# Performance work log

Measured on AMD Instinct MI355X. Metric: run time of the kernel, lower is better.

The kernel has to match this reference:

```python
import jax, jax.numpy as jnp
import numpy as np

N = 1024
BATCH = 256


def setup_inputs() -> dict:
    key = jax.random.key(0)
    k1, k2 = jax.random.split(key)
    log_alpha = jax.random.normal(k1, (BATCH, N), dtype=jnp.float32)
    W = jax.random.normal(k2, (N, N), dtype=jnp.float32)  # unnormalized transition matrix
    return {"log_alpha": log_alpha, "W": W}


def reference(log_alpha, W):
    # log_softmax over dim=0 (columns are distributions over next state)
    log_T = jax.nn.log_softmax(W, axis=0)  # [N, N]
    # log_domain_matmul: out[i, m] = logsumexp_j( log_T[i, j] + log_alpha[m, j] )
    # then transpose back -> out[m, i]
    # broadcast-add cube [BATCH, N, N] then logsumexp over j (tropical-semiring matmul)
    out = jax.scipy.special.logsumexp(
        log_T[None, :, :] + log_alpha[:, None, :], axis=2
    )  # [BATCH, N]
    return out
```

## Files before the change

kernel.cpp:

```cpp
#include <hip/hip_runtime.h>
#include <hip/hip_bf16.h>

#define N 1024
#define BATCH 256

typedef __attribute__((ext_vector_type(4))) short short4v;
typedef __attribute__((ext_vector_type(8))) short short8;
typedef __attribute__((ext_vector_type(4))) float f32x4;

static __device__ __forceinline__ ushort bfbits(float f) {
    union { __hip_bfloat16 h; ushort u; } cv; cv.h = __float2bfloat16(f); return cv.u;
}
static __device__ __forceinline__ float bf2f(ushort u) {
    union { ushort u; __hip_bfloat16 h; } cv; cv.u = u; return __bfloat162float(cv.h);
}

__global__ __launch_bounds__(256) void k1_psplit(const float* __restrict__ W,
                                                 float* __restrict__ psum,
                                                 ushort* __restrict__ Ph,
                                                 ushort* __restrict__ Pl) {
    const int t = threadIdx.x, lane = t & 63, w = t >> 6;
    const int cg = blockIdx.x & 3, slab = blockIdx.x >> 2;
    const int c = cg * 256 + lane * 4;
    __shared__ f32x4 sm[4][64];
    f32x4 acc = {0.f, 0.f, 0.f, 0.f};
#pragma unroll
    for (int it = 0; it < 4; ++it) {
        const int row = slab * 16 + w * 4 + it;
        const f32x4 v = *(const f32x4*)(W + row * N + c);
        short4v ph, pl;
        f32x4 e;
#pragma unroll
        for (int x = 0; x < 4; ++x) {
            e[x] = __expf(v[x]);
            const ushort h = bfbits(e[x]);
            ph[x] = (short)h;
            pl[x] = (short)bfbits(e[x] - bf2f(h));
        }
        *(short4v*)(Ph + row * N + c) = ph;
        *(short4v*)(Pl + row * N + c) = pl;
        acc += e;
    }
    sm[w][lane] = acc;
    __syncthreads();
    if (t < 64)
        *(f32x4*)(psum + slab * N + c) =
            sm[0][lane] + sm[1][lane] + sm[2][lane] + sm[3][lane];
}

__global__ __launch_bounds__(256) void k2_qsplit(const float* __restrict__ la,
                                                 const float* __restrict__ psum,
                                                 ushort* __restrict__ Qh,
                                                 ushort* __restrict__ Ql) {
    const int t = threadIdx.x;
    const int cg = blockIdx.x & 15, mg = blockIdx.x >> 4;
    const int c0 = cg * 64;
    __shared__ float smred[4][64];
    __shared__ float lcs[64];

    {
        const int col = t & 63, sg = t >> 6;
        float a = 0.f;
#pragma unroll
        for (int i = 0; i < 16; ++i)
            a += psum[(sg * 16 + i) * N + c0 + col];
        smred[sg][col] = a;
    }
    __syncthreads();
    if (t < 64)
        lcs[t] = __logf(smred[0][t] + smred[1][t] + smred[2][t] + smred[3][t]);
    __syncthreads();

    const int row = mg * 16 + (t >> 4);
    const int cc  = (t & 15) * 4;
    const f32x4 v = *(const f32x4*)(la + row * N + c0 + cc);
    short4v qh, ql;
#pragma unroll
    for (int x = 0; x < 4; ++x) {
        const float qv = __expf(v[x] - lcs[cc + x]);
        const ushort h = bfbits(qv);
        qh[x] = (short)h;
        ql[x] = (short)bfbits(qv - bf2f(h));
    }
    *(short4v*)(Qh + row * N + c0 + cc) = qh;
    *(short4v*)(Ql + row * N + c0 + cc) = ql;
}

__global__ __launch_bounds__(512) void k3_mm(const ushort* __restrict__ Qh,
                                             const ushort* __restrict__ Ql,
                                             const ushort* __restrict__ Ph,
                                             const ushort* __restrict__ Pl,
                                             float* __restrict__ out) {
    __shared__ f32x4 red[512];

    const int t    = threadIdx.x;
    const int lane = t & 63;
    const int wid  = t >> 6;
    const int wm   = (wid >> 1) & 1;
    const int wn   = wid & 1;
    const int g    = wid >> 2;
    const int m0   = (blockIdx.x >> 5) * 32;
    const int i0   = (blockIdx.x & 31) * 32;

    const int kb = g * 512 + (lane >> 4) * 8;
    const ushort* pAh = Qh + (m0 + wm * 16 + (lane & 15)) * N + kb;
    const ushort* pAl = Ql + (m0 + wm * 16 + (lane & 15)) * N + kb;
    const ushort* pBh = Ph + (i0 + wn * 16 + (lane & 15)) * N + kb;
    const ushort* pBl = Pl + (i0 + wn * 16 + (lane & 15)) * N + kb;

    short8 rAh[8], rAl[8], rBh[8], rBl[8];
#pragma unroll
    for (int c = 0; c < 8; ++c) {
        rAh[c] = *(const short8*)(pAh + c * 32);
        rAl[c] = *(const short8*)(pAl + c * 32);
        rBh[c] = *(const short8*)(pBh + c * 32);
        rBl[c] = *(const short8*)(pBl + c * 32);
    }

    f32x4 acc0 = {0.f, 0.f, 0.f, 0.f};
    f32x4 acc1 = {0.f, 0.f, 0.f, 0.f};

#pragma unroll
    for (int ks = 0; ks < 16; ++ks) {
        const int c = ks & 7;
        const short8 ah = rAh[c], al = rAl[c], bh = rBh[c], bl = rBl[c];
        if (ks < 8) {
            rAh[c] = *(const short8*)(pAh + (ks + 8) * 32);
            rAl[c] = *(const short8*)(pAl + (ks + 8) * 32);
            rBh[c] = *(const short8*)(pBh + (ks + 8) * 32);
            rBl[c] = *(const short8*)(pBl + (ks + 8) * 32);
        }
        if (ks & 1) {
            acc1 = __builtin_amdgcn_mfma_f32_16x16x32_bf16(ah, bh, acc1, 0, 0, 0);
            acc1 = __builtin_amdgcn_mfma_f32_16x16x32_bf16(ah, bl, acc1, 0, 0, 0);
            acc1 = __builtin_amdgcn_mfma_f32_16x16x32_bf16(al, bh, acc1, 0, 0, 0);
        } else {
            acc0 = __builtin_amdgcn_mfma_f32_16x16x32_bf16(ah, bh, acc0, 0, 0, 0);
            acc0 = __builtin_amdgcn_mfma_f32_16x16x32_bf16(ah, bl, acc0, 0, 0, 0);
            acc0 = __builtin_amdgcn_mfma_f32_16x16x32_bf16(al, bh, acc0, 0, 0, 0);
        }
    }

    red[wid * 64 + lane] = acc0 + acc1;
    __syncthreads();
    if (wid < 4) {
        const f32x4 s = red[wid * 64 + lane] + red[(wid + 4) * 64 + lane];
        const int om = m0 + wm * 16 + (lane >> 4) * 4;
        const int oi = i0 + wn * 16 + (lane & 15);
#pragma unroll
        for (int r = 0; r < 4; ++r)
            out[(om + r) * N + oi] = __logf(s[r]);
    }
}

extern "C" void kernel_launch(void* const* d_in, const int* in_sizes, int n_in,
                              void* d_out, int out_size, void* d_ws, size_t ws_size,
                              hipStream_t stream) {
    const float* la = (const float*)d_in[0];
    const float* W  = (const float*)d_in[1];
    float* out = (float*)d_out;

    char* ws = (char*)d_ws;
    float*  psum = (float*)ws;
    ushort* Ph   = (ushort*)(ws + (256 << 10));
    ushort* Pl   = Ph + (size_t)N * N;
    ushort* Qh   = Pl + (size_t)N * N;
    ushort* Ql   = Qh + (size_t)BATCH * N;

    k1_psplit<<<256, 256, 0, stream>>>(W, psum, Ph, Pl);
    k2_qsplit<<<256, 256, 0, stream>>>(la, psum, Qh, Ql);
    k3_mm<<<256, 512, 0, stream>>>(Qh, Ql, Ph, Pl, out);
}
```

Measured before the change: 78.50 us.

## Fuse three kernels into one persistent kernel with grid-wide atomic barriers

Merges the P-split, column-normalizer and MFMA matmul kernels into a single 256-block launch that synchronizes through two spin-wait atomic barriers in workspace, reset by a memset. The Q operand is no longer written to global memory: each block recomputes exp(log_alpha - lcs) and the bf16 hi/lo split inline before the MFMAs. The matmul tiling also changes to 8 waves each covering a 128-wide K chunk with a 2x2 block of 16x16 tiles, reduced through shared memory. This targets launch gaps and Q round-trip traffic, at the cost of redundant exp work across blocks and a grid barrier that depends on all 256 blocks being co-resident.

```diff
diff --git a/kernel.cpp b/kernel.cpp
--- a/kernel.cpp
+++ b/kernel.cpp
@@ -2,11 +2,12 @@
 #include <hip/hip_bf16.h>
 
 #define N 1024
-#define BATCH 256
+#define NBLK 256
 
 typedef __attribute__((ext_vector_type(4))) short short4v;
 typedef __attribute__((ext_vector_type(8))) short short8;
 typedef __attribute__((ext_vector_type(4))) float f32x4;
+typedef __attribute__((ext_vector_type(8))) float f32x8;
 
 static __device__ __forceinline__ ushort bfbits(float f) {
     union { __hip_bfloat16 h; ushort u; } cv; cv.h = __float2bfloat16(f); return cv.u;
@@ -15,138 +16,133 @@
     union { ushort u; __hip_bfloat16 h; } cv; cv.u = u; return __bfloat162float(cv.h);
 }
 
-__global__ __launch_bounds__(256) void k1_psplit(const float* __restrict__ W,
-                                                 float* __restrict__ psum,
-                                                 ushort* __restrict__ Ph,
-                                                 ushort* __restrict__ Pl) {
-    const int t = threadIdx.x, lane = t & 63, w = t >> 6;
-    const int cg = blockIdx.x & 3, slab = blockIdx.x >> 2;
-    const int c = cg * 256 + lane * 4;
-    __shared__ f32x4 sm[4][64];
-    f32x4 acc = {0.f, 0.f, 0.f, 0.f};
-#pragma unroll
-    for (int it = 0; it < 4; ++it) {
-        const int row = slab * 16 + w * 4 + it;
-        const f32x4 v = *(const f32x4*)(W + row * N + c);
-        short4v ph, pl;
-        f32x4 e;
-#pragma unroll
-        for (int x = 0; x < 4; ++x) {
-            e[x] = __expf(v[x]);
-            const ushort h = bfbits(e[x]);
-            ph[x] = (short)h;
-            pl[x] = (short)bfbits(e[x] - bf2f(h));
-        }
-        *(short4v*)(Ph + row * N + c) = ph;
-        *(short4v*)(Pl + row * N + c) = pl;
-        acc += e;
-    }
-    sm[w][lane] = acc;
-    __syncthreads();
-    if (t < 64)
-        *(f32x4*)(psum + slab * N + c) =
-            sm[0][lane] + sm[1][lane] + sm[2][lane] + sm[3][lane];
-}
+#define MFMA16(a, b, c) __builtin_amdgcn_mfma_f32_16x16x32_bf16(a, b, c, 0, 0, 0)
 
-__global__ __launch_bounds__(256) void k2_qsplit(const float* __restrict__ la,
-                                                 const float* __restrict__ psum,
-                                                 ushort* __restrict__ Qh,
-                                                 ushort* __restrict__ Ql) {
+__global__ __launch_bounds__(512, 2) void fused(const float* __restrict__ la,
+                                                const float* __restrict__ W,
+                                                float* __restrict__ out,
+                                                unsigned* __restrict__ bar,
+                                                float* __restrict__ lcs_g,
+                                                float* __restrict__ psum,
+                                                ushort* __restrict__ Ph,
+                                                ushort* __restrict__ Pl) {
+    __shared__ __align__(16) char smem_raw[8 * 64 * 4 * 16];
     const int t = threadIdx.x;
-    const int cg = blockIdx.x & 15, mg = blockIdx.x >> 4;
-    const int c0 = cg * 64;
-    __shared__ float smred[4][64];
-    __shared__ float lcs[64];
+    const int b = blockIdx.x;
 
     {
-        const int col = t & 63, sg = t >> 6;
-        float a = 0.f;
+        const int cg = b & 15, slab = b >> 4;
+        const int c4 = cg * 64 + (t & 15) * 4;
+        f32x4* smA = (f32x4*)smem_raw;
+        f32x4 part = {0.f, 0.f, 0.f, 0.f};
 #pragma unroll
-        for (int i = 0; i < 16; ++i)
-            a += psum[(sg * 16 + i) * N + c0 + col];
-        smred[sg][col] = a;
-    }
-    __syncthreads();
-    if (t < 64)
-        lcs[t] = __logf(smred[0][t] + smred[1][t] + smred[2][t] + smred[3][t]);
-    __syncthreads();
-
-    const int row = mg * 16 + (t >> 4);
-    const int cc  = (t & 15) * 4;
-    const f32x4 v = *(const f32x4*)(la + row * N + c0 + cc);
-    short4v qh, ql;
+        for (int rr = 0; rr < 2; ++rr) {
+            const int row = slab * 64 + rr * 32 + (t >> 4);
+            const f32x4 v = *(const f32x4*)(W + row * N + c4);
+            short4v ph, pl;
 #pragma unroll
-    for (int x = 0; x < 4; ++x) {
-        const float qv = __expf(v[x] - lcs[cc + x]);
-        const ushort h = bfbits(qv);
-        qh[x] = (short)h;
-        ql[x] = (short)bfbits(qv - bf2f(h));
-    }
-    *(short4v*)(Qh + row * N + c0 + cc) = qh;
-    *(short4v*)(Ql + row * N + c0 + cc) = ql;
-}
-
-__global__ __launch_bounds__(512) void k3_mm(const ushort* __restrict__ Qh,
-                                             const ushort* __restrict__ Ql,
-                                             const ushort* __restrict__ Ph,
-                                             const ushort* __restrict__ Pl,
-                                             float* __restrict__ out) {
-    __shared__ f32x4 red[512];
-
-    const int t    = threadIdx.x;
-    const int lane = t & 63;
-    const int wid  = t >> 6;
-    const int wm   = (wid >> 1) & 1;
-    const int wn   = wid & 1;
-    const int g    = wid >> 2;
-    const int m0   = (blockIdx.x >> 5) * 32;
-    const int i0   = (blockIdx.x & 31) * 32;
-
-    const int kb = g * 512 + (lane >> 4) * 8;
-    const ushort* pAh = Qh + (m0 + wm * 16 + (lane & 15)) * N + kb;
-    const ushort* pAl = Ql + (m0 + wm * 16 + (lane & 15)) * N + kb;
-    const ushort* pBh = Ph + (i0 + wn * 16 + (lane & 15)) * N + kb;
-    const ushort* pBl = Pl + (i0 + wn * 16 + (lane & 15)) * N + kb;
-
-    short8 rAh[8], rAl[8], rBh[8], rBl[8];
+            for (int x = 0; x < 4; ++x) {
+                const float e = __expf(v[x]);
+                const ushort h = bfbits(e);
+                ph[x] = (short)h;
+                pl[x] = (short)bfbits(e - bf2f(h));
+                part[x] += e;
+            }
+            *(short4v*)(Ph + row * N + c4) = ph;
+            *(short4v*)(Pl + row * N + c4) = pl;
+        }
+        smA[(t >> 4) * 16 + (t & 15)] = part;
+        __syncthreads();
+        if (t < 16) {
+            f32x4 s = smA[t];
 #pragma unroll
-    for (int c = 0; c < 8; ++c) {
-        rAh[c] = *(const short8*)(pAh + c * 32);
-        rAl[c] = *(const short8*)(pAl + c * 32);
-        rBh[c] = *(const short8*)(pBh + c * 32);
-        rBl[c] = *(const short8*)(pBl + c * 32);
-    }
-
-    f32x4 acc0 = {0.f, 0.f, 0.f, 0.f};
-    f32x4 acc1 = {0.f, 0.f, 0.f, 0.f};
-
-#pragma unroll
-    for (int ks = 0; ks < 16; ++ks) {
-        const int c = ks & 7;
-        const short8 ah = rAh[c], al = rAl[c], bh = rBh[c], bl = rBl[c];
-        if (ks < 8) {
-            rAh[c] = *(const short8*)(pAh + (ks + 8) * 32);
-            rAl[c] = *(const short8*)(pAl + (ks + 8) * 32);
-            rBh[c] = *(const short8*)(pBh + (ks + 8) * 32);
-            rBl[c] = *(const short8*)(pBl + (ks + 8) * 32);
-        }
-        if (ks & 1) {
-            acc1 = __builtin_amdgcn_mfma_f32_16x16x32_bf16(ah, bh, acc1, 0, 0, 0);
-            acc1 = __builtin_amdgcn_mfma_f32_16x16x32_bf16(ah, bl, acc1, 0, 0, 0);
-            acc1 = __builtin_amdgcn_mfma_f32_16x16x32_bf16(al, bh, acc1, 0, 0, 0);
-        } else {
-            acc0 = __builtin_amdgcn_mfma_f32_16x16x32_bf16(ah, bh, acc0, 0, 0, 0);
-            acc0 = __builtin_amdgcn_mfma_f32_16x16x32_bf16(ah, bl, acc0, 0, 0, 0);
-            acc0 = __builtin_amdgcn_mfma_f32_16x16x32_bf16(al, bh, acc0, 0, 0, 0);
+            for (int g = 1; g < 32; ++g) s += smA[g * 16 + t];
+            *(f32x4*)(psum + slab * N + cg * 64 + t * 4) = s;
         }
     }
 
-    red[wid * 64 + lane] = acc0 + acc1;
+    __syncthreads();
+    if (t == 0) {
+        __threadfence();
+        atomicAdd(&bar[0], 1u);
+        while (atomicAdd(&bar[0], 0u) < NBLK) __builtin_amdgcn_s_sleep(8);
+        __threadfence();
+    }
+    __syncthreads();
+
+    if (b < 16 && t < 64) {
+        const int c = b * 64 + t;
+        float s = 0.f;
+#pragma unroll
+        for (int sl = 0; sl < 16; ++sl) s += psum[sl * N + c];
+        lcs_g[c] = __logf(s);
+    }
+
+    __syncthreads();
+    if (t == 0) {
+        __threadfence();
+        atomicAdd(&bar[1], 1u);
+        while (atomicAdd(&bar[1], 0u) < NBLK) __builtin_amdgcn_s_sleep(8);
+        __threadfence();
+    }
+    __syncthreads();
+
+    const int lane = t & 63, wid = t >> 6;
+    const int fr = lane & 15, q = lane >> 4;
+    const int m0 = (b >> 5) * 32, i0 = (b & 31) * 32;
+    const int kc = wid * 128;
+
+    const float*  plA0 = la + (m0 + fr) * N;
+    const float*  plA1 = la + (m0 + 16 + fr) * N;
+    const ushort* pB0h = Ph + (i0 + fr) * N;
+    const ushort* pB1h = Ph + (i0 + 16 + fr) * N;
+    const ushort* pB0l = Pl + (i0 + fr) * N;
+    const ushort* pB1l = Pl + (i0 + 16 + fr) * N;
+
+    f32x4 a00 = {0.f,0.f,0.f,0.f}, a01 = {0.f,0.f,0.f,0.f};
+    f32x4 a10 = {0.f,0.f,0.f,0.f}, a11 = {0.f,0.f,0.f,0.f};
+
+#pragma unroll
+    for (int s = 0; s < 4; ++s) {
+        const int kk = kc + s * 32 + q * 8;
+        const f32x8 v0   = *(const f32x8*)(plA0 + kk);
+        const f32x8 v1   = *(const f32x8*)(plA1 + kk);
+        const f32x8 vlc  = *(const f32x8*)(lcs_g + kk);
+        const short8 b0h = *(const short8*)(pB0h + kk);
+        const short8 b1h = *(const short8*)(pB1h + kk);
+        const short8 b0l = *(const short8*)(pB0l + kk);
+        const short8 b1l = *(const short8*)(pB1l + kk);
+        short8 a0h, a0l, a1h, a1l;
+#pragma unroll
+        for (int x = 0; x < 8; ++x) {
+            const float q0 = __expf(v0[x] - vlc[x]);
+            const ushort h0 = bfbits(q0);
+            a0h[x] = (short)h0;
+            a0l[x] = (short)bfbits(q0 - bf2f(h0));
+            const float q1 = __expf(v1[x] - vlc[x]);
+            const ushort h1 = bfbits(q1);
+            a1h[x] = (short)h1;
+            a1l[x] = (short)bfbits(q1 - bf2f(h1));
+        }
+        a00 = MFMA16(a0h, b0h, a00); a00 = MFMA16(a0h, b0l, a00); a00 = MFMA16(a0l, b0h, a00);
+        a01 = MFMA16(a0h, b1h, a01); a01 = MFMA16(a0h, b1l, a01); a01 = MFMA16(a0l, b1h, a01);
+        a10 = MFMA16(a1h, b0h, a10); a10 = MFMA16(a1h, b0l, a10); a10 = MFMA16(a1l, b0h, a10);
+        a11 = MFMA16(a1h, b1h, a11); a11 = MFMA16(a1h, b1l, a11); a11 = MFMA16(a1l, b1h, a11);
+    }
+
+    __syncthreads();
+    f32x4* red = (f32x4*)smem_raw;
+    red[(wid * 64 + lane) * 4 + 0] = a00;
+    red[(wid * 64 + lane) * 4 + 1] = a01;
+    red[(wid * 64 + lane) * 4 + 2] = a10;
+    red[(wid * 64 + lane) * 4 + 3] = a11;
     __syncthreads();
     if (wid < 4) {
-        const f32x4 s = red[wid * 64 + lane] + red[(wid + 4) * 64 + lane];
-        const int om = m0 + wm * 16 + (lane >> 4) * 4;
-        const int oi = i0 + wn * 16 + (lane & 15);
+        f32x4 s = red[lane * 4 + wid];
+#pragma unroll
+        for (int w2 = 1; w2 < 8; ++w2) s += red[(w2 * 64 + lane) * 4 + wid];
+        const int om = m0 + (wid >> 1) * 16 + q * 4;
+        const int oi = i0 + (wid & 1) * 16 + fr;
 #pragma unroll
         for (int r = 0; r < 4; ++r)
             out[(om + r) * N + oi] = __logf(s[r]);
@@ -161,13 +157,12 @@
     float* out = (float*)d_out;
 
     char* ws = (char*)d_ws;
-    float*  psum = (float*)ws;
-    ushort* Ph   = (ushort*)(ws + (256 << 10));
-    ushort* Pl   = Ph + (size_t)N * N;
-    ushort* Qh   = Pl + (size_t)N * N;
-    ushort* Ql   = Qh + (size_t)BATCH * N;
+    unsigned* bar = (unsigned*)ws;
+    float* lcs_g  = (float*)(ws + 4096);
+    float* psum   = (float*)(ws + 8192);
+    ushort* Ph    = (ushort*)(ws + (128 << 10));
+    ushort* Pl    = Ph + (size_t)N * N;
 
-    k1_psplit<<<256, 256, 0, stream>>>(W, psum, Ph, Pl);
-    k2_qsplit<<<256, 256, 0, stream>>>(la, psum, Qh, Ql);
-    k3_mm<<<256, 512, 0, stream>>>(Qh, Ql, Ph, Pl, out);
+    hipMemsetAsync(bar, 0, 256, stream);
+    fused<<<NBLK, 512, 0, stream>>>(la, W, out, bar, lcs_g, psum, Ph, Pl);
 }
```

New measurement: 98.07 us. +24.9%, slower.

## Stage matmul operand tiles in LDS and share A/B fragments across waves

Applied to the files above, without the earlier changes.

The k3 matmul now copies 32x256 chunks of Qh/Ql/Ph/Pl into padded shared-memory tiles with register prefetch of the next chunk, instead of each wave loading its own fragments straight from global memory. Waves are reorganized so each covers both 16-row M halves for one N half over a 64-wide K slice, with a 4-way K-split reduction at the end. The aim is to cut redundant global/L2 traffic and raise MFMA work per loaded operand. In exchange it adds LDS traffic, two barriers per K chunk, and a larger final reduction.

```diff
diff --git a/kernel.cpp b/kernel.cpp
--- a/kernel.cpp
+++ b/kernel.cpp
@@ -3,6 +3,7 @@
 
 #define N 1024
 #define BATCH 256
+#define LP 264
 
 typedef __attribute__((ext_vector_type(4))) short short4v;
 typedef __attribute__((ext_vector_type(8))) short short8;
@@ -14,6 +15,8 @@
 static __device__ __forceinline__ float bf2f(ushort u) {
     union { ushort u; __hip_bfloat16 h; } cv; cv.u = u; return __bfloat162float(cv.h);
 }
+
+#define MFMA16(a, b, c) __builtin_amdgcn_mfma_f32_16x16x32_bf16(a, b, c, 0, 0, 0)
 
 __global__ __launch_bounds__(256) void k1_psplit(const float* __restrict__ W,
                                                  float* __restrict__ psum,
@@ -91,62 +94,84 @@
                                              const ushort* __restrict__ Ph,
                                              const ushort* __restrict__ Pl,
                                              float* __restrict__ out) {
-    __shared__ f32x4 red[512];
+    __shared__ ushort sQh[32 * LP], sQl[32 * LP];
+    __shared__ ushort sPh[32 * LP], sPl[32 * LP];
 
     const int t    = threadIdx.x;
     const int lane = t & 63;
     const int wid  = t >> 6;
-    const int wm   = (wid >> 1) & 1;
     const int wn   = wid & 1;
-    const int g    = wid >> 2;
+    const int g    = wid >> 1;
     const int m0   = (blockIdx.x >> 5) * 32;
     const int i0   = (blockIdx.x & 31) * 32;
 
-    const int kb = g * 512 + (lane >> 4) * 8;
-    const ushort* pAh = Qh + (m0 + wm * 16 + (lane & 15)) * N + kb;
-    const ushort* pAl = Ql + (m0 + wm * 16 + (lane & 15)) * N + kb;
-    const ushort* pBh = Ph + (i0 + wn * 16 + (lane & 15)) * N + kb;
-    const ushort* pBl = Pl + (i0 + wn * 16 + (lane & 15)) * N + kb;
+    const int srow = t >> 4;
+    const int skc  = (t & 15) * 8;
+    const ushort* gQh = Qh + (m0 + srow) * N + skc;
+    const ushort* gQl = Ql + (m0 + srow) * N + skc;
+    const ushort* gPh = Ph + (i0 + srow) * N + skc;
+    const ushort* gPl = Pl + (i0 + srow) * N + skc;
+    const int sd0 = srow * LP + skc;
+    const int sd1 = sd0 + 128;
 
-    short8 rAh[8], rAl[8], rBh[8], rBl[8];
-#pragma unroll
-    for (int c = 0; c < 8; ++c) {
-        rAh[c] = *(const short8*)(pAh + c * 32);
-        rAl[c] = *(const short8*)(pAl + c * 32);
-        rBh[c] = *(const short8*)(pBh + c * 32);
-        rBl[c] = *(const short8*)(pBl + c * 32);
-    }
+    const int fr  = lane & 15;
+    const int fkb = g * 64 + (lane >> 4) * 8;
+    const int a0off = (fr) * LP + fkb;
+    const int a1off = (16 + fr) * LP + fkb;
+    const int boff  = (wn * 16 + fr) * LP + fkb;
 
     f32x4 acc0 = {0.f, 0.f, 0.f, 0.f};
     f32x4 acc1 = {0.f, 0.f, 0.f, 0.f};
 
+    short8 vqh0 = *(const short8*)(gQh),       vqh1 = *(const short8*)(gQh + 128);
+    short8 vql0 = *(const short8*)(gQl),       vql1 = *(const short8*)(gQl + 128);
+    short8 vph0 = *(const short8*)(gPh),       vph1 = *(const short8*)(gPh + 128);
+    short8 vpl0 = *(const short8*)(gPl),       vpl1 = *(const short8*)(gPl + 128);
+
+    for (int k0 = 0; k0 < N; k0 += 256) {
+        __syncthreads();
+        *(short8*)&sQh[sd0] = vqh0;  *(short8*)&sQh[sd1] = vqh1;
+        *(short8*)&sQl[sd0] = vql0;  *(short8*)&sQl[sd1] = vql1;
+        *(short8*)&sPh[sd0] = vph0;  *(short8*)&sPh[sd1] = vph1;
+        *(short8*)&sPl[sd0] = vpl0;  *(short8*)&sPl[sd1] = vpl1;
+        if (k0 + 256 < N) {
+            vqh0 = *(const short8*)(gQh + k0 + 256);  vqh1 = *(const short8*)(gQh + k0 + 384);
+            vql0 = *(const short8*)(gQl + k0 + 256);  vql1 = *(const short8*)(gQl + k0 + 384);
+            vph0 = *(const short8*)(gPh + k0 + 256);  vph1 = *(const short8*)(gPh + k0 + 384);
+            vpl0 = *(const short8*)(gPl + k0 + 256);  vpl1 = *(const short8*)(gPl + k0 + 384);
+        }
+        __syncthreads();
 #pragma unroll
-    for (int ks = 0; ks < 16; ++ks) {
-        const int c = ks & 7;
-        const short8 ah = rAh[c], al = rAl[c], bh = rBh[c], bl = rBl[c];
-        if (ks < 8) {
-            rAh[c] = *(const short8*)(pAh + (ks + 8) * 32);
-            rAl[c] = *(const short8*)(pAl + (ks + 8) * 32);
-            rBh[c] = *(const short8*)(pBh + (ks + 8) * 32);
-            rBl[c] = *(const short8*)(pBl + (ks + 8) * 32);
-        }
-        if (ks & 1) {
-            acc1 = __builtin_amdgcn_mfma_f32_16x16x32_bf16(ah, bh, acc1, 0, 0, 0);
-            acc1 = __builtin_amdgcn_mfma_f32_16x16x32_bf16(ah, bl, acc1, 0, 0, 0);
-            acc1 = __builtin_amdgcn_mfma_f32_16x16x32_bf16(al, bh, acc1, 0, 0, 0);
-        } else {
-            acc0 = __builtin_amdgcn_mfma_f32_16x16x32_bf16(ah, bh, acc0, 0, 0, 0);
-            acc0 = __builtin_amdgcn_mfma_f32_16x16x32_bf16(ah, bl, acc0, 0, 0, 0);
-            acc0 = __builtin_amdgcn_mfma_f32_16x16x32_bf16(al, bh, acc0, 0, 0, 0);
+        for (int ks = 0; ks < 2; ++ks) {
+            const int so = ks * 32;
+            const short8 bh  = *(const short8*)&sPh[boff + so];
+            const short8 bl  = *(const short8*)&sPl[boff + so];
+            const short8 ah0 = *(const short8*)&sQh[a0off + so];
+            const short8 al0 = *(const short8*)&sQl[a0off + so];
+            const short8 ah1 = *(const short8*)&sQh[a1off + so];
+            const short8 al1 = *(const short8*)&sQl[a1off + so];
+            acc0 = MFMA16(ah0, bh, acc0);
+            acc0 = MFMA16(ah0, bl, acc0);
+            acc0 = MFMA16(al0, bh, acc0);
+            acc1 = MFMA16(ah1, bh, acc1);
+            acc1 = MFMA16(ah1, bl, acc1);
+            acc1 = MFMA16(al1, bh, acc1);
         }
     }
 
-    red[wid * 64 + lane] = acc0 + acc1;
+    __syncthreads();
+    f32x4* red = (f32x4*)sQh;
+    red[(wid * 64 + lane) * 2 + 0] = acc0;
+    red[(wid * 64 + lane) * 2 + 1] = acc1;
     __syncthreads();
     if (wid < 4) {
-        const f32x4 s = red[wid * 64 + lane] + red[(wid + 4) * 64 + lane];
-        const int om = m0 + wm * 16 + (lane >> 4) * 4;
-        const int oi = i0 + wn * 16 + (lane & 15);
+        const int wm_o = wid >> 1, wn_o = wid & 1;
+        f32x4 s = {0.f, 0.f, 0.f, 0.f};
+#pragma unroll
+        for (int gg = 0; gg < 4; ++gg)
+            s += red[((gg * 2 + wn_o) * 64 + lane) * 2 + wm_o];
+        const int om = m0 + wm_o * 16 + (lane >> 4) * 4;
+        const int oi = i0 + wn_o * 16 + fr;
 #pragma unroll
         for (int r = 0; r < 4; ++r)
             out[(om + r) * N + oi] = __logf(s[r]);
```

Result: faster. 68.57 us (-12.7%).
